# Kernel optimization log

Measured on AMD Instinct MI355X. Metric: run time of the kernel, lower is better.

## Reference

```python
import jax, jax.numpy as jnp
import numpy as np

GS, SO = 5, 3  # KANLinear grid_size, spline_order (efficient-kan defaults)


def kan_linear(x, base_w, spline_w, spline_scaler):
    """efficient-kan KANLinear: silu(x)@Wb^T + Bspline(x) contracted with scaled spline weights."""
    g = jnp.arange(-SO, GS + SO + 1, dtype=x.dtype) * (2.0 / GS) - 1.0  # uniform grid, len 12
    xe = x[..., None]                                                    # (..., in, 1)
    bases = ((xe >= g[:-1]) & (xe < g[1:])).astype(x.dtype)              # (..., in, 11)
    for k in range(1, SO + 1):  # Cox-de Boor recursion -> (..., in, 8)
        bases = ((xe - g[:-(k + 1)]) / (g[k:-1] - g[:-(k + 1)])) * bases[..., :-1] \
              + ((g[k + 1:] - xe) / (g[k + 1:] - g[1:-k])) * bases[..., 1:]
    out = jax.nn.silu(x) @ base_w.T
    return out + jnp.einsum('...ik,oik->...o', bases, spline_w * spline_scaler[..., None])


def reference(hidden_states, in_bw, in_sw, in_sc, conv_w, conv_b, x_bw, x_sw, x_sc,
              dt_w, dt_bias, A_logs, Ds, out_bw, out_sw, out_sc):
    B, N, L, Dm = hidden_states.shape
    d_inner, _, d_conv = conv_w.shape
    K = dt_bias.shape[0]          # 4 scan directions
    d_state = A_logs.shape[1]
    dt_rank = dt_w.shape[1]

    xz = kan_linear(hidden_states, in_bw, in_sw, in_sc)          # (B,N,L,2*Di)
    x, z = jnp.split(xz, 2, axis=-1)

    # causal depthwise conv1d + SiLU (torch pads both sides then truncates to L == left-pad)
    xc = x.reshape(B * N, L, d_inner).transpose(0, 2, 1)          # (BN,Di,L)
    xc = jax.lax.conv_general_dilated(xc, conv_w, (1,), [(d_conv - 1, 0)],
                                      dimension_numbers=('NCH', 'OIH', 'NCH'),
                                      feature_group_count=d_inner)
    xc = jax.nn.silu(xc + conv_b[None, :, None])
    x = xc.transpose(0, 2, 1).reshape(B, N, L, d_inner)

    xs = jnp.concatenate([x, jnp.flip(x, axis=2)], axis=1)        # (B,4,L,Di): fwd + seq-reversed

    x_dbl = kan_linear(xs, x_bw, x_sw, x_sc)                      # (B,4,L,R+2S)
    dt, Bs, Cs = jnp.split(x_dbl, [dt_rank, dt_rank + d_state], axis=-1)
    dts = dt @ dt_w.T                                             # (B,4,L,Di)
    delta = jax.nn.softplus(dts + dt_bias[None, :, None, :])      # (B,4,L,Di)
    A = -jnp.exp(A_logs).reshape(K, d_inner, d_state)             # (4,Di,S)

    # selective scan over L (serial data-dependent linear recurrence)
    u_t = xs.transpose(2, 0, 1, 3)      # (L,B,4,Di)
    d_t = delta.transpose(2, 0, 1, 3)   # (L,B,4,Di)
    B_t = Bs.transpose(2, 0, 1, 3)      # (L,B,4,S)
    C_t = Cs.transpose(2, 0, 1, 3)      # (L,B,4,S)

    def step(h, inp):
        u_l, dl, b_l, c_l = inp
        h = h * jnp.exp(dl[..., None] * A) + (dl * u_l)[..., None] * b_l[:, :, None, :]
        return h, jnp.einsum('bkdn,bkn->bkd', h, c_l)

    h0 = jnp.zeros((B, K, d_inner, d_state), xs.dtype)
    _, ys = jax.lax.scan(step, h0, (u_t, d_t, B_t, C_t))          # ys: (L,B,4,Di)

    y = ys.transpose(1, 2, 0, 3) + xs * Ds.reshape(K, d_inner)[None, :, None, :]  # (B,4,L,Di)
    y = y[:, :2] + jnp.flip(y[:, 2:4], axis=2)                    # merge forward/backward scans

    out = jnp.concatenate([y, z], axis=-1)                        # (B,2,L,2*Di)
    return kan_linear(out, out_bw, out_sw, out_sc)                # (B,2,L,Dm)


def setup_inputs() -> dict:
    key = jax.random.key(0)
    B, N, L = 2, 2, 1024
    d_model, d_state, d_conv, K = 512, 16, 4, 4
    d_inner = d_model            # expand=1
    dt_rank = 32                 # ceil(512/16)
    ks = jax.random.split(key, 10)

    def lin(k, o, i):
        return jax.random.normal(k, (o, i), jnp.float32) / np.sqrt(i).astype(np.float32)

    def spl(k, o, i):
        return jax.random.normal(k, (o, i, GS + SO), jnp.float32) * 0.05

    dt = jnp.exp(jax.random.uniform(ks[7], (d_inner,), jnp.float32)
                 * (np.log(0.1) - np.log(0.001)) + np.log(0.001))
    dt = jnp.clip(dt, 1e-4, None)
    inv_dt = dt + jnp.log(-jnp.expm1(-dt))

    std = dt_rank ** -0.5
    return {
        'hidden_states': jax.random.normal(ks[0], (B, N, L, d_model), jnp.float32),
        'in_bw': lin(ks[1], 2 * d_inner, d_model),
        'in_sw': spl(ks[2], 2 * d_inner, d_model),
        'in_sc': jnp.ones((2 * d_inner, d_model), jnp.float32),
        'conv_w': jax.random.normal(ks[3], (d_inner, 1, d_conv), jnp.float32) / np.sqrt(d_conv).astype(np.float32),
        'conv_b': jnp.zeros((d_inner,), jnp.float32),
        'x_bw': lin(ks[4], dt_rank + 2 * d_state, d_inner),
        'x_sw': spl(ks[5], dt_rank + 2 * d_state, d_inner),
        'x_sc': jnp.ones((dt_rank + 2 * d_state, d_inner), jnp.float32),
        'dt_w': jax.random.uniform(ks[6], (d_inner, dt_rank), jnp.float32, -std, std),
        'dt_bias': jnp.tile(inv_dt[None], (K, 1)),
        'A_logs': jnp.log(jnp.tile(jnp.arange(1, d_state + 1, dtype=jnp.float32)[None], (K * d_inner, 1))),
        'Ds': jnp.ones((K * d_inner,), jnp.float32),
        'out_bw': lin(ks[8], d_model, 2 * d_inner),
        'out_sw': spl(ks[9], d_model, 2 * d_inner),
        'out_sc': jnp.ones((d_model, 2 * d_inner), jnp.float32),
    }
```

## Files before the change

kernel.cpp:

```cpp
#include <hip/hip_runtime.h>
#include <stdint.h>

#define DEV __device__ __forceinline__

typedef __attribute__((ext_vector_type(8))) short short8;
typedef __attribute__((ext_vector_type(4))) float f32x4;

DEV unsigned short f2bf(float f) {
    union { float f; uint32_t u; } v; v.f = f;
    uint32_t u = v.u;
    return (unsigned short)((u + 0x7fffu + ((u >> 16) & 1u)) >> 16);
}
DEV float silu_f(float x) { return x / (1.0f + __expf(-x)); }

DEV void bspline8(float x, float* bo) {
    float b[11];
#pragma unroll
    for (int j = 0; j < 11; ++j) {
        float gj  = 0.4f * (float)(j - 3) - 1.0f;
        float gj1 = 0.4f * (float)(j - 2) - 1.0f;
        b[j] = (x >= gj && x < gj1) ? 1.0f : 0.0f;
    }
#pragma unroll
    for (int k = 1; k <= 3; ++k) {
        float inv = 1.0f / (0.4f * (float)k);
#pragma unroll
        for (int j = 0; j + k < 11; ++j) {
            float gj  = 0.4f * (float)(j - 3) - 1.0f;
            float gk1 = 0.4f * (float)(j + k - 2) - 1.0f;
            b[j] = ((x - gj) * b[j] + (gk1 - x) * b[j + 1]) * inv;
        }
    }
#pragma unroll
    for (int j = 0; j < 8; ++j) bo[j] = b[j];
}

__global__ __launch_bounds__(256) void zero_kernel(float4* __restrict__ p, int n4) {
    int i = blockIdx.x * 256 + threadIdx.x;
    if (i < n4) p[i] = make_float4(0.f, 0.f, 0.f, 0.f);
}

__global__ __launch_bounds__(256) void add3_kernel(float4* __restrict__ dst,
        const float4* __restrict__ s1, const float4* __restrict__ s2, int n4) {
    int i = blockIdx.x * 256 + threadIdx.x;
    if (i >= n4) return;
    float4 d = dst[i], a = s1[i], b = s2[i];
    d.x += a.x + b.x; d.y += a.y + b.y; d.z += a.z + b.z; d.w += a.w + b.w;
    dst[i] = d;
}

__global__ __launch_bounds__(256) void wc8_kernel(const float* __restrict__ bw,
        const float* __restrict__ sw, const float* __restrict__ sc,
        unsigned short* __restrict__ Wc, int total) {
    int g = (blockIdx.x * 256 + threadIdx.x) * 8;
    if (g >= total) return;
    float bwv[8], scv[8], swv[64];
    *(float4*)&bwv[0] = *(const float4*)&bw[g];
    *(float4*)&bwv[4] = *(const float4*)&bw[g + 4];
    *(float4*)&scv[0] = *(const float4*)&sc[g];
    *(float4*)&scv[4] = *(const float4*)&sc[g + 4];
#pragma unroll
    for (int q = 0; q < 16; ++q) *(float4*)&swv[q * 4] = *(const float4*)&sw[(size_t)g * 8 + q * 4];
    unsigned short buf[72];
#pragma unroll
    for (int e = 0; e < 8; ++e) {
        buf[e * 9] = f2bf(bwv[e]);
#pragma unroll
        for (int j = 0; j < 8; ++j) buf[e * 9 + 1 + j] = f2bf(swv[e * 8 + j] * scv[e]);
    }
    unsigned short* o = Wc + (size_t)g * 9;
#pragma unroll
    for (int q = 0; q < 9; ++q) *(short8*)&o[q * 8] = *(short8*)&buf[q * 8];
}

__global__ __launch_bounds__(256) void feat8_kernel(const float* __restrict__ X,
        unsigned short* __restrict__ F, int total) {
    int g = (blockIdx.x * 256 + threadIdx.x) * 8;
    if (g >= total) return;
    float xv[8];
    *(float4*)&xv[0] = *(const float4*)&X[g];
    *(float4*)&xv[4] = *(const float4*)&X[g + 4];
    unsigned short buf[72];
#pragma unroll
    for (int e = 0; e < 8; ++e) {
        float x = xv[e];
        buf[e * 9] = f2bf(silu_f(x));
        float bo[8];
        bspline8(x, bo);
#pragma unroll
        for (int j = 0; j < 8; ++j) buf[e * 9 + 1 + j] = f2bf(bo[j]);
    }
    unsigned short* o = F + (size_t)g * 9;
#pragma unroll
    for (int q = 0; q < 9; ++q) *(short8*)&o[q * 8] = *(short8*)&buf[q * 8];
}

template<int BM, int BN, int DEPTH, bool ATOMIC>
__global__ __launch_bounds__(256) void gemm_mfma2(const unsigned short* __restrict__ A,
        const unsigned short* __restrict__ B, float* __restrict__ C0,
        float* __restrict__ C1, float* __restrict__ C2,
        int M, int N, int K, int klen, int gx, int gy, int gz) {
    constexpr int NB  = DEPTH + 2;
    constexpr int FRM = BM / 32;
    constexpr int FRN = BN / 32;
    constexpr int GLA = (BM * 64) / 4096;
    constexpr int GLB = (BN * 64) / 4096;
    constexpr int GL  = GLA + GLB;
    constexpr int LDA = BM * 32;
    constexpr int LDB = BN * 32;
    __shared__ unsigned short As[NB * LDA];
    __shared__ unsigned short Bs[NB * LDB];

    const int nwg = gx * gy * gz;
    int fid = (blockIdx.z * gy + blockIdx.y) * gx + blockIdx.x;
    int cpx = nwg >> 3;
    fid = (fid & 7) * cpx + (fid >> 3);
    const int bx = fid % gx;
    const int by = (fid / gx) % gy;
    const int bz = fid / (gx * gy);

    const int tid = threadIdx.x;
    const int lane = tid & 63;
    const int w = tid >> 6;
    const int wr = w >> 1, wc = w & 1;
    const int bm = bx * BM, bn = by * BN;
    const int kbase = bz * klen;
    const int NT = klen / 32;
    const int frow = lane & 15;
    const int uq = ((lane >> 4) ^ ((frow >> 1) & 3)) * 8;

    float* __restrict__ C = (bz == 0) ? C0 : (bz == 1) ? C1 : C2;

    f32x4 acc[FRM][FRN];
#pragma unroll
    for (int m = 0; m < FRM; ++m)
#pragma unroll
        for (int n = 0; n < FRN; ++n)
            acc[m][n] = (f32x4){0.f, 0.f, 0.f, 0.f};

    auto stage = [&](int t, int buf) {
        const int k0 = kbase + t * 32;
#pragma unroll
        for (int r = 0; r < GLA; ++r) {
            int bo = r * 4096 + tid * 16;
            int row = bo >> 6;
            int lu = ((bo >> 4) & 3) ^ ((row >> 1) & 3);
            __builtin_amdgcn_global_load_lds(
                (const __attribute__((address_space(1))) void*)((const char*)A + ((size_t)(bm + row) * K + k0) * 2 + lu * 16),
                (__attribute__((address_space(3))) void*)((char*)As + (size_t)buf * LDA * 2 + bo), 16, 0, 0);
        }
#pragma unroll
        for (int r = 0; r < GLB; ++r) {
            int bo = r * 4096 + tid * 16;
            int row = bo >> 6;
            int lu = ((bo >> 4) & 3) ^ ((row >> 1) & 3);
            __builtin_amdgcn_global_load_lds(
                (const __attribute__((address_space(1))) void*)((const char*)B + ((size_t)(bn + row) * K + k0) * 2 + lu * 16),
                (__attribute__((address_space(3))) void*)((char*)Bs + (size_t)buf * LDB * 2 + bo), 16, 0, 0);
        }
    };

    auto compute = [&](int buf) {
        const unsigned short* as = As + (size_t)buf * LDA;
        const unsigned short* bs = Bs + (size_t)buf * LDB;
        short8 af[FRM], bf[FRN];
#pragma unroll
        for (int m = 0; m < FRM; ++m)
            af[m] = *(const short8*)&as[(wr * (BM / 2) + m * 16 + frow) * 32 + uq];
#pragma unroll
        for (int n = 0; n < FRN; ++n)
            bf[n] = *(const short8*)&bs[(wc * (BN / 2) + n * 16 + frow) * 32 + uq];
#pragma unroll
        for (int m = 0; m < FRM; ++m)
#pragma unroll
            for (int n = 0; n < FRN; ++n)
                acc[m][n] = __builtin_amdgcn_mfma_f32_16x16x32_bf16(af[m], bf[n], acc[m][n], 0, 0, 0);
    };

    for (int t = 0; t < DEPTH; ++t) stage(t, t);

    int rb = 0, sb = DEPTH;
    int t = 0;
    for (; t + DEPTH < NT; ++t) {
        stage(t + DEPTH, sb);
        asm volatile("s_waitcnt vmcnt(%0)" :: "i"(DEPTH * GL) : "memory");
        asm volatile("s_barrier" ::: "memory");
        compute(rb);
        rb = (rb + 1 == NB) ? 0 : rb + 1;
        sb = (sb + 1 == NB) ? 0 : sb + 1;
    }
    for (; t < NT; ++t) {
        asm volatile("s_waitcnt vmcnt(0)" ::: "memory");
        asm volatile("s_barrier" ::: "memory");
        compute(rb);
        rb = (rb + 1 == NB) ? 0 : rb + 1;
    }

    const int crow = (lane >> 4) * 4;
    const int ccol = lane & 15;
#pragma unroll
    for (int m = 0; m < FRM; ++m)
#pragma unroll
        for (int n = 0; n < FRN; ++n) {
            int gr = bm + wr * (BM / 2) + m * 16 + crow;
            int gc = bn + wc * (BN / 2) + n * 16 + ccol;
#pragma unroll
            for (int r = 0; r < 4; ++r) {
                if (ATOMIC) atomicAdd(&C[(size_t)(gr + r) * N + gc], acc[m][n][r]);
                else        C[(size_t)(gr + r) * N + gc] = acc[m][n][r];
            }
        }
}

__global__ __launch_bounds__(256) void conv_xs_kernel(const float* __restrict__ xz,
        const float* __restrict__ cw, const float* __restrict__ cb,
        float* __restrict__ xs) {
    int idx = blockIdx.x * 256 + threadIdx.x;
    int d = idx & 511;
    int l = (idx >> 9) & 1023;
    int bn = idx >> 19;
    const float* xcol = xz + (size_t)(bn * 1024) * 1024 + d;
    float acc = cb[d];
#pragma unroll
    for (int h = 0; h < 4; ++h) {
        int ls = l - 3 + h;
        float xv = (ls >= 0) ? xcol[(size_t)ls * 1024] : 0.0f;
        acc = fmaf(cw[d * 4 + h], xv, acc);
    }
    float v = silu_f(acc);
    int b = bn >> 1, nn = bn & 1;
    xs[((size_t)(b * 4 + nn) * 1024 + l) * 512 + d] = v;
    xs[((size_t)(b * 4 + nn + 2) * 1024 + (1023 - l)) * 512 + d] = v;
}

__global__ __launch_bounds__(256) void delta_kernel(const float* __restrict__ xdbl,
        const float* __restrict__ dtw, const float* __restrict__ dtb,
        float* __restrict__ delta) {
    int t = blockIdx.x >> 1;
    int half = blockIdx.x & 1;
    int d = half * 256 + threadIdx.x;
    __shared__ float dtv[32];
    if (threadIdx.x < 32) dtv[threadIdx.x] = xdbl[(size_t)t * 64 + threadIdx.x];
    __syncthreads();
    const float* w = dtw + (size_t)d * 32;
    float acc = 0.0f;
#pragma unroll
    for (int r = 0; r < 32; r += 4) {
        float4 wv = *(const float4*)(w + r);
        acc = fmaf(dtv[r], wv.x, acc);
        acc = fmaf(dtv[r + 1], wv.y, acc);
        acc = fmaf(dtv[r + 2], wv.z, acc);
        acc = fmaf(dtv[r + 3], wv.w, acc);
    }
    int k = (t >> 10) & 3;
    float x = acc + dtb[k * 512 + d];
    float sp = (x > 20.0f) ? x : log1pf(__expf(x));
    delta[(size_t)t * 512 + d] = sp;
}

__global__ __launch_bounds__(256) void scanA_kernel(const float* __restrict__ delta,
        const float* __restrict__ xs, const float* __restrict__ xdbl,
        const float* __restrict__ A_logs, float* __restrict__ P, float* __restrict__ Q) {
    int half = blockIdx.x & 1;
    int chunk = (blockIdx.x >> 1) & 15;
    int bk = blockIdx.x >> 5;
    int k = bk & 3;
    int d = half * 256 + threadIdx.x;
    __shared__ float Bl[64][16];
    for (int s = threadIdx.x; s < 64 * 16; s += 256) {
        int ll = s >> 4, n = s & 15;
        Bl[ll][n] = xdbl[(size_t)(bk * 1024 + chunk * 64 + ll) * 64 + 32 + n];
    }
    __syncthreads();
    float An[16];
#pragma unroll
    for (int n = 0; n < 16; ++n) An[n] = -__expf(A_logs[(size_t)(k * 512 + d) * 16 + n]);
    float h[16] = {};
    float p[16];
#pragma unroll
    for (int n = 0; n < 16; ++n) p[n] = 1.0f;
    int base = bk * 1024 + chunk * 64;
    for (int ll = 0; ll < 64; ++ll) {
        size_t off = (size_t)(base + ll) * 512 + d;
        float da = delta[off];
        float du = da * xs[off];
#pragma unroll
        for (int n = 0; n < 16; ++n) {
            float a = __expf(da * An[n]);
            h[n] = fmaf(h[n], a, du * Bl[ll][n]);
            p[n] *= a;
        }
    }
    size_t pb = ((size_t)(bk * 16 + chunk) * 16) * 512 + d;
#pragma unroll
    for (int n = 0; n < 16; ++n) { P[pb + n * 512] = p[n]; Q[pb + n * 512] = h[n]; }
}

__global__ __launch_bounds__(512) void scanB_kernel(const float* __restrict__ P,
        const float* __restrict__ Q, float* __restrict__ Hst) {
    int bk = blockIdx.x >> 4;
    int n  = blockIdx.x & 15;
    int d  = threadIdx.x;
    float h = 0.0f;
    for (int chunk = 0; chunk < 16; ++chunk) {
        size_t base = ((size_t)((bk * 16 + chunk) * 16 + n)) * 512 + d;
        Hst[base] = h;
        h = fmaf(P[base], h, Q[base]);
    }
}

__global__ __launch_bounds__(256) void scanC_kernel(const float* __restrict__ delta,
        float* __restrict__ xs, const float* __restrict__ xdbl,
        const float* __restrict__ A_logs, const float* __restrict__ Hst,
        const float* __restrict__ Ds) {
    int half = blockIdx.x & 1;
    int chunk = (blockIdx.x >> 1) & 15;
    int bk = blockIdx.x >> 5;
    int k = bk & 3;
    int d = half * 256 + threadIdx.x;
    __shared__ float BC[64][32];
    for (int s = threadIdx.x; s < 64 * 32; s += 256) {
        int ll = s >> 5, n = s & 31;
        BC[ll][n] = xdbl[(size_t)(bk * 1024 + chunk * 64 + ll) * 64 + 32 + n];
    }
    __syncthreads();
    float An[16];
#pragma unroll
    for (int n = 0; n < 16; ++n) An[n] = -__expf(A_logs[(size_t)(k * 512 + d) * 16 + n]);
    float h[16];
    size_t hb = ((size_t)(bk * 16 + chunk) * 16) * 512 + d;
#pragma unroll
    for (int n = 0; n < 16; ++n) h[n] = Hst[hb + n * 512];
    float Dv = Ds[k * 512 + d];
    int base = bk * 1024 + chunk * 64;
    for (int ll = 0; ll < 64; ++ll) {
        size_t off = (size_t)(base + ll) * 512 + d;
        float da = delta[off];
        float u = xs[off];
        float du = da * u;
        float y = 0.0f;
#pragma unroll
        for (int n = 0; n < 16; ++n) {
            float a = __expf(da * An[n]);
            h[n] = fmaf(h[n], a, du * BC[ll][n]);
            y = fmaf(h[n], BC[ll][16 + n], y);
        }
        xs[off] = fmaf(u, Dv, y);
    }
}

__global__ __launch_bounds__(256) void merge_kernel(const float* __restrict__ ys,
        float* __restrict__ xz) {
    int idx = blockIdx.x * 256 + threadIdx.x;
    int d = idx & 511;
    int l = (idx >> 9) & 1023;
    int nn = (idx >> 19) & 1;
    int b = idx >> 20;
    float v = ys[((size_t)(b * 4 + nn) * 1024 + l) * 512 + d]
            + ys[((size_t)(b * 4 + nn + 2) * 1024 + (1023 - l)) * 512 + d];
    size_t trow = (size_t)(b * 2 + nn) * 1024 + l;
    xz[trow * 1024 + d] = v;
}

extern "C" void kernel_launch(void* const* d_in, const int* in_sizes, int n_in,
                              void* d_out, int out_size, void* d_ws, size_t ws_size,
                              hipStream_t stream) {
    const float* hidden  = (const float*)d_in[0];
    const float* in_bw   = (const float*)d_in[1];
    const float* in_sw   = (const float*)d_in[2];
    const float* in_sc   = (const float*)d_in[3];
    const float* conv_w  = (const float*)d_in[4];
    const float* conv_b  = (const float*)d_in[5];
    const float* x_bw    = (const float*)d_in[6];
    const float* x_sw    = (const float*)d_in[7];
    const float* x_sc    = (const float*)d_in[8];
    const float* dt_w    = (const float*)d_in[9];
    const float* dt_bias = (const float*)d_in[10];
    const float* A_logs  = (const float*)d_in[11];
    const float* Ds      = (const float*)d_in[12];
    const float* out_bw  = (const float*)d_in[13];
    const float* out_sw  = (const float*)d_in[14];
    const float* out_sc  = (const float*)d_in[15];
    float* out = (float*)d_out;
    char* ws = (char*)d_ws;

    float* XZ    = (float*)(ws + 0);
    float* XS    = (float*)(ws + 16777216);
    float* XDBL  = (float*)(ws + 33554432);
    unsigned short* FEAT = (unsigned short*)(ws + 35651584);
    float* DELTA = (float*)(ws + 35651584);
    float* P     = (float*)(ws + 52428800);
    float* Q     = (float*)(ws + 56623104);
    float* HST   = (float*)(ws + 60817408);
    float* XZP1  = (float*)(ws + 73400320);
    float* XZP2  = (float*)(ws + 90177536);
    float* OP1   = (float*)(ws + 16777216);
    float* OP2   = (float*)(ws + 16777216 + 8388608);
    unsigned short* WCbuf = (unsigned short*)(ws + 111149056);
    unsigned short* WC2   = (unsigned short*)(ws + 120586240);

    wc8_kernel<<<256, 256, 0, stream>>>(in_bw, in_sw, in_sc, WCbuf, 1024 * 512);
    wc8_kernel<<<16, 256, 0, stream>>>(x_bw, x_sw, x_sc, WC2, 64 * 512);

    feat8_kernel<<<1024, 256, 0, stream>>>(hidden, FEAT, 4096 * 512);
    gemm_mfma2<128, 128, 1, false><<<dim3(32, 8, 3), 256, 0, stream>>>(
        FEAT, WCbuf, XZ, XZP1, XZP2, 4096, 1024, 4608, 1536, 32, 8, 3);
    add3_kernel<<<4096, 256, 0, stream>>>((float4*)XZ, (const float4*)XZP1, (const float4*)XZP2, (4096 * 1024) / 4);

    wc8_kernel<<<256, 256, 0, stream>>>(out_bw, out_sw, out_sc, WCbuf, 512 * 1024);

    conv_xs_kernel<<<8192, 256, 0, stream>>>(XZ, conv_w, conv_b, XS);

    feat8_kernel<<<2048, 256, 0, stream>>>(XS, FEAT, 8192 * 512);
    zero_kernel<<<512, 256, 0, stream>>>((float4*)XDBL, (8192 * 64) / 4);
    gemm_mfma2<64, 64, 1, true><<<dim3(128, 1, 4), 256, 0, stream>>>(
        FEAT, WC2, XDBL, XDBL, XDBL, 8192, 64, 4608, 1152, 128, 1, 4);

    delta_kernel<<<16384, 256, 0, stream>>>(XDBL, dt_w, dt_bias, DELTA);

    scanA_kernel<<<256, 256, 0, stream>>>(DELTA, XS, XDBL, A_logs, P, Q);
    scanB_kernel<<<128, 512, 0, stream>>>(P, Q, HST);
    scanC_kernel<<<256, 256, 0, stream>>>(DELTA, XS, XDBL, A_logs, HST, Ds);

    merge_kernel<<<8192, 256, 0, stream>>>(XS, XZ);

    feat8_kernel<<<2048, 256, 0, stream>>>(XZ, FEAT, 4096 * 1024);
    gemm_mfma2<128, 128, 1, false><<<dim3(32, 4, 3), 256, 0, stream>>>(
        FEAT, WCbuf, out, OP1, OP2, 4096, 512, 9216, 3072, 32, 4, 3);
    add3_kernel<<<2048, 256, 0, stream>>>((float4*)out, (const float4*)OP1, (const float4*)OP2, (4096 * 512) / 4);
}
```

Baseline: 534.6 us.

## Deduplicate reversed-direction work and fuse softplus into scan kernels

The conv output is no longer materialised twice (forward and flipped). The x_proj KAN GEMM, feature expansion and dt projection now run on 4096 tokens instead of 8192, since the flipped directions are the same per-token values; the scan kernels index the shared buffer through a token-remapping helper. Softplus and the dt bias move into scanA/scanC, so the delta buffer is no longer written and re-read. The scan chunk length drops from 64 to 32, giving twice as many blocks, and the output GEMM tile changes to 128x64 for more workgroups. In exchange the scan reads reversed-direction rows in reverse token order and recomputes softplus in both scan passes.

After: 486.8 us. -9.0%, faster.

```diff
diff --git a/kernel.cpp b/kernel.cpp
--- a/kernel.cpp
+++ b/kernel.cpp
@@ -12,6 +12,14 @@
     return (unsigned short)((u + 0x7fffu + ((u >> 16) & 1u)) >> 16);
 }
 DEV float silu_f(float x) { return x / (1.0f + __expf(-x)); }
+DEV float softplus_f(float x) { return (x > 20.0f) ? x : log1pf(__expf(x)); }
+
+DEV int tokx(int bk, int l) {
+    int b = bk >> 2;
+    int nn = bk & 1;
+    int lf = (bk & 2) ? (1023 - l) : l;
+    return (b * 2 + nn) * 1024 + lf;
+}
 
 DEV void bspline8(float x, float* bo) {
     float b[11];
@@ -214,7 +222,7 @@
 
 __global__ __launch_bounds__(256) void conv_xs_kernel(const float* __restrict__ xz,
         const float* __restrict__ cw, const float* __restrict__ cb,
-        float* __restrict__ xs) {
+        float* __restrict__ xsb) {
     int idx = blockIdx.x * 256 + threadIdx.x;
     int d = idx & 511;
     int l = (idx >> 9) & 1023;
@@ -227,15 +235,11 @@
         float xv = (ls >= 0) ? xcol[(size_t)ls * 1024] : 0.0f;
         acc = fmaf(cw[d * 4 + h], xv, acc);
     }
-    float v = silu_f(acc);
-    int b = bn >> 1, nn = bn & 1;
-    xs[((size_t)(b * 4 + nn) * 1024 + l) * 512 + d] = v;
-    xs[((size_t)(b * 4 + nn + 2) * 1024 + (1023 - l)) * 512 + d] = v;
-}
-
-__global__ __launch_bounds__(256) void delta_kernel(const float* __restrict__ xdbl,
-        const float* __restrict__ dtw, const float* __restrict__ dtb,
-        float* __restrict__ delta) {
+    xsb[((size_t)bn * 1024 + l) * 512 + d] = silu_f(acc);
+}
+
+__global__ __launch_bounds__(256) void dts_kernel(const float* __restrict__ xdbl,
+        const float* __restrict__ dtw, float* __restrict__ dts) {
     int t = blockIdx.x >> 1;
     int half = blockIdx.x & 1;
     int d = half * 256 + threadIdx.x;
@@ -252,38 +256,36 @@
         acc = fmaf(dtv[r + 2], wv.z, acc);
         acc = fmaf(dtv[r + 3], wv.w, acc);
     }
-    int k = (t >> 10) & 3;
-    float x = acc + dtb[k * 512 + d];
-    float sp = (x > 20.0f) ? x : log1pf(__expf(x));
-    delta[(size_t)t * 512 + d] = sp;
-}
-
-__global__ __launch_bounds__(256) void scanA_kernel(const float* __restrict__ delta,
-        const float* __restrict__ xs, const float* __restrict__ xdbl,
-        const float* __restrict__ A_logs, float* __restrict__ P, float* __restrict__ Q) {
+    dts[(size_t)t * 512 + d] = acc;
+}
+
+__global__ __launch_bounds__(256) void scanA_kernel(const float* __restrict__ dts,
+        const float* __restrict__ xsb, const float* __restrict__ xdbl,
+        const float* __restrict__ A_logs, const float* __restrict__ dtb,
+        float* __restrict__ P, float* __restrict__ Q) {
     int half = blockIdx.x & 1;
-    int chunk = (blockIdx.x >> 1) & 15;
-    int bk = blockIdx.x >> 5;
+    int chunk = (blockIdx.x >> 1) & 31;
+    int bk = blockIdx.x >> 6;
     int k = bk & 3;
     int d = half * 256 + threadIdx.x;
-    __shared__ float Bl[64][16];
-    for (int s = threadIdx.x; s < 64 * 16; s += 256) {
+    __shared__ float Bl[32][16];
+    for (int s = threadIdx.x; s < 32 * 16; s += 256) {
         int ll = s >> 4, n = s & 15;
-        Bl[ll][n] = xdbl[(size_t)(bk * 1024 + chunk * 64 + ll) * 64 + 32 + n];
+        Bl[ll][n] = xdbl[(size_t)tokx(bk, chunk * 32 + ll) * 64 + 32 + n];
     }
     __syncthreads();
     float An[16];
 #pragma unroll
     for (int n = 0; n < 16; ++n) An[n] = -__expf(A_logs[(size_t)(k * 512 + d) * 16 + n]);
+    float bias = dtb[k * 512 + d];
     float h[16] = {};
     float p[16];
 #pragma unroll
     for (int n = 0; n < 16; ++n) p[n] = 1.0f;
-    int base = bk * 1024 + chunk * 64;
-    for (int ll = 0; ll < 64; ++ll) {
-        size_t off = (size_t)(base + ll) * 512 + d;
-        float da = delta[off];
-        float du = da * xs[off];
+    for (int ll = 0; ll < 32; ++ll) {
+        size_t off = (size_t)tokx(bk, chunk * 32 + ll) * 512 + d;
+        float da = softplus_f(dts[off] + bias);
+        float du = da * xsb[off];
 #pragma unroll
         for (int n = 0; n < 16; ++n) {
             float a = __expf(da * An[n]);
@@ -291,7 +293,7 @@
             p[n] *= a;
         }
     }
-    size_t pb = ((size_t)(bk * 16 + chunk) * 16) * 512 + d;
+    size_t pb = ((size_t)(bk * 32 + chunk) * 16) * 512 + d;
 #pragma unroll
     for (int n = 0; n < 16; ++n) { P[pb + n * 512] = p[n]; Q[pb + n * 512] = h[n]; }
 }
@@ -302,41 +304,43 @@
     int n  = blockIdx.x & 15;
     int d  = threadIdx.x;
     float h = 0.0f;
-    for (int chunk = 0; chunk < 16; ++chunk) {
-        size_t base = ((size_t)((bk * 16 + chunk) * 16 + n)) * 512 + d;
+    for (int chunk = 0; chunk < 32; ++chunk) {
+        size_t base = ((size_t)((bk * 32 + chunk) * 16 + n)) * 512 + d;
         Hst[base] = h;
         h = fmaf(P[base], h, Q[base]);
     }
 }
 
-__global__ __launch_bounds__(256) void scanC_kernel(const float* __restrict__ delta,
-        float* __restrict__ xs, const float* __restrict__ xdbl,
-        const float* __restrict__ A_logs, const float* __restrict__ Hst,
-        const float* __restrict__ Ds) {
+__global__ __launch_bounds__(256) void scanC_kernel(const float* __restrict__ dts,
+        const float* __restrict__ xsb, const float* __restrict__ xdbl,
+        const float* __restrict__ A_logs, const float* __restrict__ dtb,
+        const float* __restrict__ Hst, const float* __restrict__ Ds,
+        float* __restrict__ ys) {
     int half = blockIdx.x & 1;
-    int chunk = (blockIdx.x >> 1) & 15;
-    int bk = blockIdx.x >> 5;
+    int chunk = (blockIdx.x >> 1) & 31;
+    int bk = blockIdx.x >> 6;
     int k = bk & 3;
     int d = half * 256 + threadIdx.x;
-    __shared__ float BC[64][32];
-    for (int s = threadIdx.x; s < 64 * 32; s += 256) {
+    __shared__ float BC[32][32];
+    for (int s = threadIdx.x; s < 32 * 32; s += 256) {
         int ll = s >> 5, n = s & 31;
-        BC[ll][n] = xdbl[(size_t)(bk * 1024 + chunk * 64 + ll) * 64 + 32 + n];
+        BC[ll][n] = xdbl[(size_t)tokx(bk, chunk * 32 + ll) * 64 + 32 + n];
     }
     __syncthreads();
     float An[16];
 #pragma unroll
     for (int n = 0; n < 16; ++n) An[n] = -__expf(A_logs[(size_t)(k * 512 + d) * 16 + n]);
+    float bias = dtb[k * 512 + d];
     float h[16];
-    size_t hb = ((size_t)(bk * 16 + chunk) * 16) * 512 + d;
+    size_t hb = ((size_t)(bk * 32 + chunk) * 16) * 512 + d;
 #pragma unroll
     for (int n = 0; n < 16; ++n) h[n] = Hst[hb + n * 512];
     float Dv = Ds[k * 512 + d];
-    int base = bk * 1024 + chunk * 64;
-    for (int ll = 0; ll < 64; ++ll) {
-        size_t off = (size_t)(base + ll) * 512 + d;
-        float da = delta[off];
-        float u = xs[off];
+    for (int ll = 0; ll < 32; ++ll) {
+        int l = chunk * 32 + ll;
+        size_t off = (size_t)tokx(bk, l) * 512 + d;
+        float da = softplus_f(dts[off] + bias);
+        float u = xsb[off];
         float du = da * u;
         float y = 0.0f;
 #pragma unroll
@@ -345,7 +349,7 @@
             h[n] = fmaf(h[n], a, du * BC[ll][n]);
             y = fmaf(h[n], BC[ll][16 + n], y);
         }
-        xs[off] = fmaf(u, Dv, y);
+        ys[((size_t)bk * 1024 + l) * 512 + d] = fmaf(u, Dv, y);
     }
 }
 
@@ -385,19 +389,21 @@
     char* ws = (char*)d_ws;
 
     float* XZ    = (float*)(ws + 0);
-    float* XS    = (float*)(ws + 16777216);
-    float* XDBL  = (float*)(ws + 33554432);
-    unsigned short* FEAT = (unsigned short*)(ws + 35651584);
-    float* DELTA = (float*)(ws + 35651584);
-    float* P     = (float*)(ws + 52428800);
-    float* Q     = (float*)(ws + 56623104);
-    float* HST   = (float*)(ws + 60817408);
-    float* XZP1  = (float*)(ws + 73400320);
-    float* XZP2  = (float*)(ws + 90177536);
+    float* XSB   = (float*)(ws + 16777216);
+    float* XDBL  = (float*)(ws + 25165824);
+    float* DTS   = (float*)(ws + 26214400);
+    char*  zone  = ws + 34603008;
+    unsigned short* FEAT = (unsigned short*)zone;
+    float* YS    = (float*)zone;
+    float* P     = (float*)(zone + 16777216);
+    float* Q     = (float*)(zone + 25165824);
+    float* HST   = (float*)(zone + 33554432);
+    float* XZP1  = (float*)(zone + 37748736);
+    float* XZP2  = (float*)(zone + 54525952);
     float* OP1   = (float*)(ws + 16777216);
-    float* OP2   = (float*)(ws + 16777216 + 8388608);
-    unsigned short* WCbuf = (unsigned short*)(ws + 111149056);
-    unsigned short* WC2   = (unsigned short*)(ws + 120586240);
+    float* OP2   = (float*)(ws + 26214400);
+    unsigned short* WCbuf = (unsigned short*)(ws + 110100480);
+    unsigned short* WC2   = (unsigned short*)(ws + 119537664);
 
     wc8_kernel<<<256, 256, 0, stream>>>(in_bw, in_sw, in_sc, WCbuf, 1024 * 512);
     wc8_kernel<<<16, 256, 0, stream>>>(x_bw, x_sw, x_sc, WC2, 64 * 512);
@@ -409,23 +415,23 @@
 
     wc8_kernel<<<256, 256, 0, stream>>>(out_bw, out_sw, out_sc, WCbuf, 512 * 1024);
 
-    conv_xs_kernel<<<8192, 256, 0, stream>>>(XZ, conv_w, conv_b, XS);
-
-    feat8_kernel<<<2048, 256, 0, stream>>>(XS, FEAT, 8192 * 512);
-    zero_kernel<<<512, 256, 0, stream>>>((float4*)XDBL, (8192 * 64) / 4);
-    gemm_mfma2<64, 64, 1, true><<<dim3(128, 1, 4), 256, 0, stream>>>(
-        FEAT, WC2, XDBL, XDBL, XDBL, 8192, 64, 4608, 1152, 128, 1, 4);
-
-    delta_kernel<<<16384, 256, 0, stream>>>(XDBL, dt_w, dt_bias, DELTA);
-
-    scanA_kernel<<<256, 256, 0, stream>>>(DELTA, XS, XDBL, A_logs, P, Q);
+    conv_xs_kernel<<<8192, 256, 0, stream>>>(XZ, conv_w, conv_b, XSB);
+
+    feat8_kernel<<<1024, 256, 0, stream>>>(XSB, FEAT, 4096 * 512);
+    zero_kernel<<<256, 256, 0, stream>>>((float4*)XDBL, (4096 * 64) / 4);
+    gemm_mfma2<64, 64, 1, true><<<dim3(64, 1, 8), 256, 0, stream>>>(
+        FEAT, WC2, XDBL, XDBL, XDBL, 4096, 64, 4608, 576, 64, 1, 8);
+
+    dts_kernel<<<8192, 256, 0, stream>>>(XDBL, dt_w, DTS);
+
+    scanA_kernel<<<512, 256, 0, stream>>>(DTS, XSB, XDBL, A_logs, dt_bias, P, Q);
     scanB_kernel<<<128, 512, 0, stream>>>(P, Q, HST);
-    scanC_kernel<<<256, 256, 0, stream>>>(DELTA, XS, XDBL, A_logs, HST, Ds);
-
-    merge_kernel<<<8192, 256, 0, stream>>>(XS, XZ);
+    scanC_kernel<<<512, 256, 0, stream>>>(DTS, XSB, XDBL, A_logs, dt_bias, HST, Ds, YS);
+
+    merge_kernel<<<8192, 256, 0, stream>>>(YS, XZ);
 
     feat8_kernel<<<2048, 256, 0, stream>>>(XZ, FEAT, 4096 * 1024);
-    gemm_mfma2<128, 128, 1, false><<<dim3(32, 4, 3), 256, 0, stream>>>(
-        FEAT, WCbuf, out, OP1, OP2, 4096, 512, 9216, 3072, 32, 4, 3);
+    gemm_mfma2<128, 64, 1, false><<<dim3(32, 8, 3), 256, 0, stream>>>(
+        FEAT, WCbuf, out, OP1, OP2, 4096, 512, 9216, 3072, 32, 8, 3);
     add3_kernel<<<2048, 256, 0, stream>>>((float4*)out, (const float4*)OP1, (const float4*)OP2, (4096 * 512) / 4);
 }
```
